# Kernel tuning notes

Measured on AMD Instinct MI355X. Metric: run time of the kernel, lower is better.

## Reference

```python
import jax, jax.numpy as jnp
import numpy as np

B, T, N, H, L, KS = 8, 1024, 64, 8, 2, 3  # batch, seq_len, num_features(=graph n), heads, blocks, Cheb order
D1 = 64  # tq MLP hidden (hardcoded 64 in original)
EPS = 1e-6


def setup_inputs() -> dict:
    key = jax.random.key(0)
    ks = jax.random.split(key, 30)
    def nrm(k, shp, sc=0.05):
        return jax.random.normal(k, shp, dtype=jnp.float32) * sc
    return {
        "inputs": jax.random.normal(ks[0], (B, T, N), dtype=jnp.float32),
        "pos_emb": nrm(ks[1], (T, N)),
        "K3": nrm(ks[2], (N, KS, N), 0.1),  # Chebyshev kernel Lk reshaped [n, Ks, n] (constant)
        "qw": nrm(ks[3], (L, H, KS)), "qb": nrm(ks[4], (L, H)),
        "kw": nrm(ks[5], (L, H, KS)), "kb": nrm(ks[6], (L, H)),
        "vw": nrm(ks[7], (L, H, KS)), "vb": nrm(ks[8], (L, H)),
        "tqW1": nrm(ks[9], (L, H, T, D1)), "tqb1": nrm(ks[10], (L, H, D1)),
        "tqW2": nrm(ks[11], (L, H, D1, D1)), "tqb2": nrm(ks[12], (L, H, D1)),
        "tqW3": nrm(ks[13], (L, H, D1, 2)), "tqb3": nrm(ks[14], (L, H, 2)),
        "Wlt": nrm(ks[15], (L, H * N, N)),
        "ln1g": jnp.ones((L, N), jnp.float32), "ln1b": jnp.zeros((L, N), jnp.float32),
        "ln2g": jnp.ones((L, N), jnp.float32), "ln2b": jnp.zeros((L, N), jnp.float32),
        "sclw": nrm(ks[16], (L, KS)), "sclb": nrm(ks[17], (L,)),
        "elW": nrm(ks[18], (L, N, N)), "elb": nrm(ks[19], (L, N)),
        "fW1": nrm(ks[20], (N, 32)), "fb1": nrm(ks[21], (32,)),
        "fW2": nrm(ks[22], (32, 1)), "fb2": nrm(ks[23], (1,)),
    }


def _ln(x, g, b):
    m = jnp.mean(x, axis=-1, keepdims=True)
    v = jnp.mean((x - m) ** 2, axis=-1, keepdims=True)
    return (x - m) * jax.lax.rsqrt(v + EPS) * g + b


def _head_gconv(x, K3, ws, bs):
    # SpatialConvLayer (c_in=c_out=1) per head: relu(sum_k ws[h,k]*(x @ L_k) + bs[h] + x)
    g = jnp.einsum('btn,nkm,hk->bhtm', x, K3, ws) + bs[None, :, None, None]
    return jax.nn.relu(g + x[:, None])  # [B,H,T,N]


def reference(inputs, pos_emb, K3, qw, qb, kw, kb, vw, vb, tqW1, tqb1, tqW2, tqb2,
              tqW3, tqb3, Wlt, ln1g, ln1b, ln2g, ln2b, sclw, sclb, elW, elb,
              fW1, fb1, fW2, fb2):
    x = inputs + pos_emb  # position embedding layer
    for l in range(L):
        xq = _head_gconv(x, K3, qw[l], qb[l])
        xk = _head_gconv(x, K3, kw[l], kb[l])
        xv = _head_gconv(x, K3, vw[l], vb[l])
        # s_a[b,t,s] = sum_n xk[b,t,n] * xq[b,s,n], scaled by 1/num_features
        s = jnp.einsum('bhtn,bhsn->bhts', xk, xq) / N
        sft = jax.nn.softmax(s, axis=-1)
        # talking-quantity gate: MLP over rows of transposed softmax matrix
        p = jnp.swapaxes(sft, -1, -2)  # [B,H,T,T]
        h1 = jax.nn.relu(jnp.einsum('bhts,hsd->bhtd', p, tqW1[l]) + tqb1[l][None, :, None, :])
        h2 = jax.nn.relu(jnp.einsum('bhtd,hde->bhte', h1, tqW2[l]) + tqb2[l][None, :, None, :])
        g = jax.nn.softmax(jnp.einsum('bhtd,hde->bhte', h2, tqW3[l]) + tqb3[l][None, :, None, :], axis=-1)  # [B,H,T,2]
        auv = jnp.einsum('bhts,bhsn->bhtn', sft, xv)
        ho = g[..., 0:1] * auv + g[..., 1:2] * xv  # gated mix, [B,H,T,N]
        a_x = jnp.transpose(ho, (0, 2, 1, 3)).reshape(B, T, H * N)  # head concat
        out1 = _ln(x + a_x @ Wlt[l], ln1g[l], ln1b[l])  # dropout omitted (inference)
        gc = jnp.einsum('btn,nkm,k->btm', out1, K3, sclw[l]) + sclb[l]
        ffn = jax.nn.relu(gc + out1)  # SpatialConvLayer residual relu
        ffn = ffn @ elW[l] + elb[l]
        x = _ln(out1 + ffn, ln2g[l], ln2b[l])
    pooled = jnp.mean(x, axis=1)  # GlobalAveragePooling1D
    h = jax.nn.relu(pooled @ fW1 + fb1)
    return h @ fW2 + fb2  # [B,1]
```

## Files before the change

### kernel.cpp

```cpp
#include <hip/hip_runtime.h>

typedef __attribute__((ext_vector_type(8))) short short8;
typedef __attribute__((ext_vector_type(4))) float f32x4;

#define BB 8
#define TT 1024
#define NN 64
#define HH 8
#define LL 2
#define KSS 3
#define DD1 64
#define EPSV 1e-6f
#define LOG2E 1.4426950408889634f

#define MFMA16(a, b, c) __builtin_amdgcn_mfma_f32_16x16x32_bf16(a, b, c, 0, 0, 0)
#define BAR() __builtin_amdgcn_s_barrier()
#define WAIT_VM8() asm volatile("s_waitcnt vmcnt(8)" ::: "memory")
#define WAIT_VM2() asm volatile("s_waitcnt vmcnt(2)" ::: "memory")
#define WAIT_VM0() asm volatile("s_waitcnt vmcnt(0)" ::: "memory")
#define WAIT_LGKM0() asm volatile("s_waitcnt lgkmcnt(0)" ::: "memory")

__device__ __forceinline__ float exp2_(float x) { return __builtin_amdgcn_exp2f(x); }
__device__ __forceinline__ float log2_(float x) { return __builtin_amdgcn_logf(x); }

__device__ __forceinline__ void split1(float x, ushort& hi, ushort& lo) {
  uint u = __float_as_uint(x);
  hi = (ushort)(u >> 16);
  float hf = __uint_as_float(u & 0xffff0000u);
  lo = (ushort)(__float_as_uint(x - hf) >> 16);
}
__device__ __forceinline__ uint pack2(float a, float b, uint& lo) {
  uint ua = __float_as_uint(a), ub = __float_as_uint(b);
  float ra = __uint_as_float(ua & 0xffff0000u);
  float rb = __uint_as_float(ub & 0xffff0000u);
  lo = (__float_as_uint(a - ra) >> 16) | (__float_as_uint(b - rb) & 0xffff0000u);
  return (ua >> 16) | (ub & 0xffff0000u);
}
__device__ __forceinline__ uint pack2rhu(float a, float b) {
  uint ua = __float_as_uint(a) + 0x8000u;
  uint ub = __float_as_uint(b) + 0x8000u;
  return (ua >> 16) | (ub & 0xffff0000u);
}
__device__ __forceinline__ ushort f2bfr(float x) {
  union { float f; uint u; } v; v.f = x;
  uint r = (v.u + 0x7fffu + ((v.u >> 16) & 1u)) >> 16;
  return (ushort)r;
}
__device__ __forceinline__ float bf2f(ushort b) {
  union { uint u; float f; } v; v.u = ((uint)b) << 16; return v.f;
}

__device__ __forceinline__ void gl2lds16(const ushort* g, ushort* l) {
  __builtin_amdgcn_global_load_lds(
      (const __attribute__((address_space(1))) void*)g,
      (__attribute__((address_space(3))) void*)l, 16, 0, 0);
}
__device__ __forceinline__ void stage_async(ushort* __restrict__ s,
                                            const ushort* __restrict__ g,
                                            int stride, int tid) {
  int w = tid >> 6;
  int sub = (tid & 63) >> 3, c = tid & 7;
#pragma unroll
  for (int i = 0; i < 2; ++i) {
    int rb = (i * 4 + w) * 8;
    gl2lds16(g + (size_t)(rb + sub) * stride + ((c ^ sub) << 3), s + rb * 64);
  }
}
__device__ __forceinline__ short8 frag(const ushort* __restrict__ s, int row, int ch) {
  return *(const short8*)(s + row * 64 + ((ch ^ (row & 7)) << 3));
}
__device__ __forceinline__ void stage_q32(ushort* __restrict__ s,
                                          const ushort* __restrict__ g, int tid) {
  int w = tid >> 6;
  int sub = (tid & 63) >> 3, c = tid & 7;
  int rb = w * 8, r = rb + sub;
  gl2lds16(g + (size_t)r * 64 + ((c ^ (r & 7)) << 3), s + rb * 64);
}
__device__ __forceinline__ void stage_v32(ushort* __restrict__ s,
                                          const ushort* __restrict__ g, int tid) {
  int w = tid >> 6;
  int noff = (tid & 63) >> 2, c = tid & 3;
  int nb = w * 16, n = nb + noff;
  gl2lds16(g + (size_t)n * 1024 + ((c ^ ((n >> 1) & 3)) << 3), s + nb * 32);
}
__device__ __forceinline__ short8 frag32(const ushort* __restrict__ s, int row, int g) {
  return *(const short8*)(s + row * 32 + ((g ^ ((row >> 1) & 3)) << 3));
}


__global__ void k_addpos(const float* __restrict__ in, const float* __restrict__ pe,
                         float* __restrict__ x, int total) {
  int idx = blockIdx.x * 256 + threadIdx.x;
  if (idx < total) {
    int tn = idx & (TT * NN - 1);
    x[idx] = in[idx] + pe[tn];
  }
}

__global__ void k_k3s(const float* __restrict__ K3, const float* __restrict__ sclwl,
                      ushort* __restrict__ dh) {
  int idx = blockIdx.x * 256 + threadIdx.x;
  int n = idx >> 6, m = idx & 63;
  float v = K3[n * 192 + m] * sclwl[0] + K3[n * 192 + 64 + m] * sclwl[1] +
            K3[n * 192 + 128 + m] * sclwl[2];
  dh[m * 64 + n] = f2bfr(v);
}

__global__ __launch_bounds__(256) void k_tsplit(const float* __restrict__ src,
                                                ushort* __restrict__ dh) {
  __shared__ float st[64][65];
  int blk = blockIdx.x;
  int mat = blk >> 4, rt = blk & 15;
  int tid = threadIdx.x;
  size_t sbase = ((size_t)mat * TT + rt * 64) * 64;
#pragma unroll
  for (int i = 0; i < 4; ++i) {
    int idx = tid + i * 256;
    int r = idx >> 4, c4 = idx & 15;
    float4 v = *(const float4*)(src + sbase + r * 64 + c4 * 4);
    st[r][c4 * 4 + 0] = v.x; st[r][c4 * 4 + 1] = v.y;
    st[r][c4 * 4 + 2] = v.z; st[r][c4 * 4 + 3] = v.w;
  }
  __syncthreads();
  size_t obase = (size_t)mat * (64 * (size_t)TT) + rt * 64;
#pragma unroll
  for (int i = 0; i < 2; ++i) {
    int idx = tid + i * 256;
    int n = idx >> 3, c = idx & 7;
    uint hw[4];
#pragma unroll
    for (int j = 0; j < 4; ++j)
      hw[j] = (uint)f2bfr(st[c * 8 + 2 * j][n]) | ((uint)f2bfr(st[c * 8 + 2 * j + 1][n]) << 16);
    *(uint4*)(dh + obase + (size_t)n * TT + c * 8) = make_uint4(hw[0], hw[1], hw[2], hw[3]);
  }
}

__global__ __launch_bounds__(256) void k_tsplitW(const float* __restrict__ Wlt,
                                                 ushort* __restrict__ dh,
                                                 ushort* __restrict__ dl) {
  __shared__ float st[64][65];
  int blk = blockIdx.x;
  int l = blk >> 3, rt = blk & 7;
  int tid = threadIdx.x;
  size_t sbase = ((size_t)l * 512 + rt * 64) * 64;
#pragma unroll
  for (int i = 0; i < 4; ++i) {
    int idx = tid + i * 256;
    int r = idx >> 4, c4 = idx & 15;
    float4 v = *(const float4*)(Wlt + sbase + r * 64 + c4 * 4);
    st[r][c4 * 4 + 0] = v.x; st[r][c4 * 4 + 1] = v.y;
    st[r][c4 * 4 + 2] = v.z; st[r][c4 * 4 + 3] = v.w;
  }
  __syncthreads();
  size_t obase = (size_t)l * 64 * 512 + rt * 64;
#pragma unroll
  for (int i = 0; i < 2; ++i) {
    int idx = tid + i * 256;
    int n = idx >> 3, c = idx & 7;
    uint hw[4], lw[4];
#pragma unroll
    for (int j = 0; j < 4; ++j) hw[j] = pack2(st[c * 8 + 2 * j][n], st[c * 8 + 2 * j + 1][n], lw[j]);
    *(uint4*)(dh + obase + (size_t)n * 512 + c * 8) = make_uint4(hw[0], hw[1], hw[2], hw[3]);
    *(uint4*)(dl + obase + (size_t)n * 512 + c * 8) = make_uint4(lw[0], lw[1], lw[2], lw[3]);
  }
}

__global__ __launch_bounds__(256) void k_tsplitSq(const float* __restrict__ src,
                                                  ushort* __restrict__ dh) {
  __shared__ float st[64][65];
  int mat = blockIdx.x;
  int tid = threadIdx.x;
  size_t sbase = (size_t)mat * 4096;
#pragma unroll
  for (int i = 0; i < 4; ++i) {
    int idx = tid + i * 256;
    int r = idx >> 4, c4 = idx & 15;
    float4 v = *(const float4*)(src + sbase + r * 64 + c4 * 4);
    st[r][c4 * 4 + 0] = v.x; st[r][c4 * 4 + 1] = v.y;
    st[r][c4 * 4 + 2] = v.z; st[r][c4 * 4 + 3] = v.w;
  }
  __syncthreads();
#pragma unroll
  for (int i = 0; i < 2; ++i) {
    int idx = tid + i * 256;
    int d = idx >> 3, c = idx & 7;
    uint hw[4];
#pragma unroll
    for (int j = 0; j < 4; ++j)
      hw[j] = (uint)f2bfr(st[c * 8 + 2 * j][d]) | ((uint)f2bfr(st[c * 8 + 2 * j + 1][d]) << 16);
    *(uint4*)(dh + sbase + (size_t)d * 64 + c * 8) = make_uint4(hw[0], hw[1], hw[2], hw[3]);
  }
}

__global__ __launch_bounds__(256) void k_gconv(
    const float* __restrict__ x, const float* __restrict__ K3,
    const float* __restrict__ qwl, const float* __restrict__ qbl,
    const float* __restrict__ kwl, const float* __restrict__ kbl,
    const float* __restrict__ vwl, const float* __restrict__ vbl,
    ushort* __restrict__ xqh, ushort* __restrict__ xkh, float* __restrict__ xv) {
  __shared__ float sK3[12288];
  __shared__ float sx[4][64];
  int tid = threadIdx.x;
  int w = tid >> 6, lane = tid & 63;
#pragma unroll
  for (int i = 0; i < 12; ++i)
    ((float4*)sK3)[tid + i * 256] = ((const float4*)K3)[tid + i * 256];
  size_t bt = (size_t)blockIdx.x * 4 + w;
  size_t b = bt >> 10, t = bt & 1023;
  float xm = x[bt * 64 + lane];
  sx[w][lane] = xm;
  __syncthreads();
  float a0 = 0.f, a1 = 0.f, a2 = 0.f;
#pragma unroll 8
  for (int n = 0; n < 64; ++n) {
    float xn = sx[w][n];
    a0 = fmaf(xn, sK3[n * 192 + lane], a0);
    a1 = fmaf(xn, sK3[n * 192 + 64 + lane], a1);
    a2 = fmaf(xn, sK3[n * 192 + 128 + lane], a2);
  }
#pragma unroll
  for (int hh = 0; hh < HH; ++hh) {
    size_t off = (((size_t)b * HH + hh) * TT + t) * 64 + lane;
    float q = fmaf(qwl[hh * 3 + 0], a0,
              fmaf(qwl[hh * 3 + 1], a1, fmaf(qwl[hh * 3 + 2], a2, qbl[hh] + xm)));
    q = fmaxf(q, 0.f) * (0.015625f * LOG2E);
    xqh[off] = f2bfr(q);
    float k = fmaf(kwl[hh * 3 + 0], a0,
              fmaf(kwl[hh * 3 + 1], a1, fmaf(kwl[hh * 3 + 2], a2, kbl[hh] + xm)));
    xkh[off] = f2bfr(fmaxf(k, 0.f));
    float v = fmaf(vwl[hh * 3 + 0], a0,
              fmaf(vwl[hh * 3 + 1], a1, fmaf(vwl[hh * 3 + 2], a2, vbl[hh] + xm)));
    xv[off] = fmaxf(v, 0.f);
  }
}

__global__ __launch_bounds__(256, 4) void k_attn(
    const ushort* __restrict__ xkh, const ushort* __restrict__ xqh,
    const ushort* __restrict__ xvTh,
    float* __restrict__ auv, float* __restrict__ lse) {
  __shared__ ushort sQh[4096];
  __shared__ ushort sVh[4096];
  __shared__ ushort sPh[2048];
  int tid = threadIdx.x;
  int lane = tid & 63, w = tid >> 6;
  int l15 = lane & 15, g = lane >> 4;
  int nb = gridDim.x, chunk = nb >> 3, bid = blockIdx.x;
  int blk = (bid & 7) * chunk + (bid >> 3);
  int bh = blk >> 4, t0 = (blk & 15) << 6;
  size_t bhTT = (size_t)bh * TT;
  int trow = 16 * w + l15, psw = (trow >> 1) & 3;

  stage_async(sQh, xkh + (bhTT + t0) * NN, 64, tid);
  WAIT_VM0();
  BAR();
  short8 fKh[2];
#pragma unroll
  for (int ks = 0; ks < 2; ++ks) fKh[ks] = frag(sQh, trow, g + 4 * ks);
  WAIT_LGKM0();
  BAR();
  stage_q32(sQh, xqh + bhTT * NN, tid);
  stage_v32(sVh, xvTh + bhTT * NN, tid);
  stage_q32(sQh + 2048, xqh + (bhTT + 32) * NN, tid);
  stage_v32(sVh + 2048, xvTh + bhTT * NN + 32, tid);

  float lsum = 0.f;
  f32x4 O[4];
#pragma unroll
  for (int ct = 0; ct < 4; ++ct)
#pragma unroll
    for (int r = 0; r < 4; ++r) O[ct][r] = 0.f;

  for (int ut = 0; ut < 32; ++ut) {
    int cur = ut & 1;
    if (ut < 31) WAIT_VM2(); else WAIT_VM0();
    BAR();
    const ushort* cQh = sQh + cur * 2048;
    const ushort* cVh = sVh + cur * 2048;

    __builtin_amdgcn_s_setprio(1);
    f32x4 S[2];
#pragma unroll
    for (int rt = 0; rt < 2; ++rt) {
      f32x4 a = {0.f, 0.f, 0.f, 0.f};
#pragma unroll
      for (int ks = 0; ks < 2; ++ks)
        a = MFMA16(frag(cQh, 16 * rt + l15, g + 4 * ks), fKh[ks], a);
      S[rt] = a;
    }
    __builtin_amdgcn_s_setprio(0);

    uint2 ph[2];
#pragma unroll
    for (int rt = 0; rt < 2; ++rt) {
      float p0 = exp2_(S[rt][0]), p1 = exp2_(S[rt][1]);
      float p2 = exp2_(S[rt][2]), p3 = exp2_(S[rt][3]);
      lsum += (p0 + p1) + (p2 + p3);
      ph[rt].x = pack2rhu(p0, p1);
      ph[rt].y = pack2rhu(p2, p3);
    }
#pragma unroll
    for (int rt = 0; rt < 2; ++rt) {
      int ch = 2 * rt + (g >> 1);
      int off = trow * 32 + ((ch ^ psw) << 3) + ((g & 1) << 2);
      *(uint2*)(sPh + off) = ph[rt];
    }
    WAIT_LGKM0();
    __builtin_amdgcn_sched_barrier(0);
    __builtin_amdgcn_s_setprio(1);
    {
      short8 aPh = frag32(sPh, trow, g);
#pragma unroll
      for (int ct = 0; ct < 4; ++ct)
        O[ct] = MFMA16(aPh, frag32(cVh, 16 * ct + l15, g), O[ct]);
    }
    __builtin_amdgcn_s_setprio(0);
    WAIT_LGKM0();
    BAR();
    if (ut < 30) {
      int tn = ut + 2;
      stage_q32(sQh + cur * 2048, xqh + (bhTT + tn * 32) * NN, tid);
      stage_v32(sVh + cur * 2048, xvTh + bhTT * NN + tn * 32, tid);
    }
  }
  lsum += __shfl_xor(lsum, 16, 64);
  lsum += __shfl_xor(lsum, 32, 64);
  float il = 1.0f / lsum;
  float ilr[4];
#pragma unroll
  for (int r = 0; r < 4; ++r) ilr[r] = __shfl(il, (lane & 48) | (4 * g + r), 64);
#pragma unroll
  for (int r = 0; r < 4; ++r) {
    size_t row = (bhTT + t0 + 16 * w + 4 * g + r) * NN;
#pragma unroll
    for (int ct = 0; ct < 4; ++ct) auv[row + 16 * ct + l15] = O[ct][r] * ilr[r];
  }
  if (g == 0) lse[bhTT + t0 + trow] = log2_(lsum);
}

__global__ __launch_bounds__(256, 4) void k_h1g(
    const ushort* __restrict__ xkh, const ushort* __restrict__ xqh,
    const ushort* __restrict__ w1Th, const float* __restrict__ lse,
    const float* __restrict__ b1, const ushort* __restrict__ w2Th,
    const float* __restrict__ b2l, const float* __restrict__ W3l,
    const float* __restrict__ b3l, const float* __restrict__ auv,
    const float* __restrict__ xv, ushort* __restrict__ hoh,
    ushort* __restrict__ hol) {
  __shared__ ushort sKh[4096];
  __shared__ ushort sWh[4096];
  __shared__ ushort sPh[2048];
  __shared__ ushort sW2[4096];
  __shared__ float sL[1024];
  int tid = threadIdx.x;
  int lane = tid & 63, w = tid >> 6;
  int l15 = lane & 15, g = lane >> 4;
  int nb = gridDim.x, chunk = nb >> 3, bid = blockIdx.x;
  int blk = (bid & 7) * chunk + (bid >> 3);
  int bh = blk >> 4, h = bh & (HH - 1), a0 = (blk & 15) << 6;
  size_t bhTT = (size_t)bh * TT;
  size_t wbase = (size_t)h * NN * TT;
  int arow = 16 * w + l15, psw = (arow >> 1) & 3;

  stage_async(sKh, xqh + (bhTT + a0) * NN, 64, tid);
  stage_async(sW2, w2Th + (size_t)h * 4096, 64, tid);
  WAIT_VM0();
  BAR();
  short8 fQh[2];
#pragma unroll
  for (int ks = 0; ks < 2; ++ks) fQh[ks] = frag(sKh, arow, g + 4 * ks);
#pragma unroll
  for (int i = 0; i < 4; ++i) sL[tid + i * 256] = lse[bhTT + tid + i * 256];
  WAIT_LGKM0();
  BAR();
  stage_q32(sKh, xkh + bhTT * NN, tid);
  stage_v32(sWh, w1Th + wbase, tid);
  stage_q32(sKh + 2048, xkh + (bhTT + 32) * NN, tid);
  stage_v32(sWh + 2048, w1Th + wbase + 32, tid);

  f32x4 acc[4];
#pragma unroll
  for (int ct = 0; ct < 4; ++ct)
#pragma unroll
    for (int r = 0; r < 4; ++r) acc[ct][r] = 0.f;

  for (int tt = 0; tt < 32; ++tt) {
    int cur = tt & 1;
    if (tt < 31) WAIT_VM2(); else WAIT_VM0();
    BAR();
    const ushort* cKh = sKh + cur * 2048;
    const ushort* cWh = sWh + cur * 2048;

    __builtin_amdgcn_s_setprio(1);
    f32x4 S[2];
#pragma unroll
    for (int rt = 0; rt < 2; ++rt) {
      f32x4 a = {0.f, 0.f, 0.f, 0.f};
#pragma unroll
      for (int ks = 0; ks < 2; ++ks)
        a = MFMA16(frag(cKh, 16 * rt + l15, g + 4 * ks), fQh[ks], a);
      S[rt] = a;
    }
    __builtin_amdgcn_s_setprio(0);

    uint2 ph[2];
#pragma unroll
    for (int rt = 0; rt < 2; ++rt) {
      f32x4 lv = *(const f32x4*)(sL + tt * 32 + 16 * rt + 4 * g);
      float p0 = exp2_(S[rt][0] - lv[0]);
      float p1 = exp2_(S[rt][1] - lv[1]);
      float p2 = exp2_(S[rt][2] - lv[2]);
      float p3 = exp2_(S[rt][3] - lv[3]);
      ph[rt].x = pack2rhu(p0, p1);
      ph[rt].y = pack2rhu(p2, p3);
    }
#pragma unroll
    for (int rt = 0; rt < 2; ++rt) {
      int ch = 2 * rt + (g >> 1);
      int off = arow * 32 + ((ch ^ psw) << 3) + ((g & 1) << 2);
      *(uint2*)(sPh + off) = ph[rt];
    }
    WAIT_LGKM0();
    __builtin_amdgcn_sched_barrier(0);
    __builtin_amdgcn_s_setprio(1);
    {
      short8 aPh = frag32(sPh, arow, g);
#pragma unroll
      for (int ct = 0; ct < 4; ++ct)
        acc[ct] = MFMA16(aPh, frag32(cWh, 16 * ct + l15, g), acc[ct]);
    }
    __builtin_amdgcn_s_setprio(0);
    WAIT_LGKM0();
    BAR();
    if (tt < 30) {
      int tn = tt + 2;
      stage_q32(sKh + cur * 2048, xkh + (bhTT + tn * 32) * NN, tid);
      stage_v32(sWh + cur * 2048, w1Th + wbase + tn * 32, tid);
    }
  }
#pragma unroll
  for (int ct = 0; ct < 4; ++ct) {
    float bb = b1[h * 64 + 16 * ct + l15];
    int cch = 2 * ct + (l15 >> 3), cin = l15 & 7;
#pragma unroll
    for (int r = 0; r < 4; ++r) {
      int row = 16 * w + 4 * g + r;
      float hv = fmaxf(acc[ct][r] + bb, 0.f);
      sWh[row * 64 + ((cch ^ (row & 7)) << 3) + cin] = f2bfr(hv);
    }
  }
  WAIT_LGKM0();
  BAR();
  f32x4 acc2[4];
#pragma unroll
  for (int rt = 0; rt < 4; ++rt)
#pragma unroll
    for (int r = 0; r < 4; ++r) acc2[rt][r] = 0.f;
#pragma unroll
  for (int ks = 0; ks < 2; ++ks) {
    short8 bB = frag(sW2, 16 * w + l15, g + 4 * ks);
#pragma unroll
    for (int rt = 0; rt < 4; ++rt)
      acc2[rt] = MFMA16(frag(sWh, 16 * rt + l15, g + 4 * ks), bB, acc2[rt]);
  }
  int col = 16 * w + l15;
  float b2c = b2l[h * 64 + col];
  float w30 = W3l[h * 128 + col * 2 + 0];
  float w31 = W3l[h * 128 + col * 2 + 1];
  float* sredf = sL;
  float* sgf = sL + 512;
#pragma unroll
  for (int rt = 0; rt < 4; ++rt)
#pragma unroll
    for (int r = 0; r < 4; ++r) {
      float v = fmaxf(acc2[rt][r] + b2c, 0.f);
      float z0 = v * w30, z1 = v * w31;
#pragma unroll
      for (int mm = 1; mm < 16; mm <<= 1) {
        z0 += __shfl_xor(z0, mm, 64);
        z1 += __shfl_xor(z1, mm, 64);
      }
      if (l15 == 0) {
        int row = 16 * rt + 4 * g + r;
        sredf[row * 4 + w] = z0;
        sredf[256 + row * 4 + w] = z1;
      }
    }
  __syncthreads();
  if (tid < 64) {
    float z0 = sredf[tid * 4] + sredf[tid * 4 + 1] + sredf[tid * 4 + 2] +
               sredf[tid * 4 + 3] + b3l[h * 2 + 0];
    float z1 = sredf[256 + tid * 4] + sredf[256 + tid * 4 + 1] +
               sredf[256 + tid * 4 + 2] + sredf[256 + tid * 4 + 3] + b3l[h * 2 + 1];
    float g0 = 1.0f / (1.0f + __expf(z1 - z0));
    sgf[tid * 2] = g0;
    sgf[tid * 2 + 1] = 1.0f - g0;
  }
  __syncthreads();
#pragma unroll
  for (int rr = 0; rr < 16; ++rr) {
    int row = 16 * w + rr;
    size_t off = (bhTT + a0 + row) * 64 + lane;
    float ho = sgf[row * 2] * auv[off] + sgf[row * 2 + 1] * xv[off];
    ushort hb, lb;
    split1(ho, hb, lb);
    hoh[off] = hb;
    hol[off] = lb;
  }
}

__global__ __launch_bounds__(256, 2) void k_mrgf(
    float* __restrict__ x, const ushort* __restrict__ hoh,
    const ushort* __restrict__ hol, const ushort* __restrict__ wth,
    const ushort* __restrict__ wtl, const float* __restrict__ g1l,
    const float* __restrict__ b1l, const float* __restrict__ sclb_l,
    const ushort* __restrict__ k3sTh, const ushort* __restrict__ elWTh,
    const float* __restrict__ elbl, const float* __restrict__ g2l,
    const float* __restrict__ b2l) {
  __shared__ ushort sAh[2][4096], sAl[2][4096], sBh[2][4096], sBl[2][4096];
  __shared__ float sred[2][64][4];
  __shared__ float sfin[64][2];
  int tid = threadIdx.x;
  int lane = tid & 63, w = tid >> 6;
  int l15 = lane & 15, g = lane >> 4;
  int blk = blockIdx.x;
  int b = blk >> 4, t0 = (blk & 15) << 6;

  {
    size_t ab0 = (((size_t)b * HH + 0) * TT + t0) * NN;
    size_t ab1 = (((size_t)b * HH + 1) * TT + t0) * NN;
    stage_async(sAh[0], hoh + ab0, 64, tid);
    stage_async(sAl[0], hol + ab0, 64, tid);
    stage_async(sBh[0], wth, 512, tid);
    stage_async(sBl[0], wtl, 512, tid);
    stage_async(sAh[1], hoh + ab1, 64, tid);
    stage_async(sAl[1], hol + ab1, 64, tid);
    stage_async(sBh[1], wth + 64, 512, tid);
    stage_async(sBl[1], wtl + 64, 512, tid);
  }

  f32x4 acc[4];
#pragma unroll
  for (int rt = 0; rt < 4; ++rt)
#pragma unroll
    for (int r = 0; r < 4; ++r) acc[rt][r] = 0.f;

  for (int h = 0; h < 8; ++h) {
    int cur = h & 1;
    if (h < 7) WAIT_VM8(); else WAIT_VM0();
    BAR();
    __builtin_amdgcn_s_setprio(1);
#pragma unroll
    for (int ks = 0; ks < 2; ++ks) {
      short8 bBh = frag(sBh[cur], 16 * w + l15, g + 4 * ks);
      short8 bBl = frag(sBl[cur], 16 * w + l15, g + 4 * ks);
#pragma unroll
      for (int rt = 0; rt < 4; ++rt) {
        short8 aAh = frag(sAh[cur], 16 * rt + l15, g + 4 * ks);
        short8 aAl = frag(sAl[cur], 16 * rt + l15, g + 4 * ks);
        acc[rt] = MFMA16(aAh, bBh, acc[rt]);
        acc[rt] = MFMA16(aAh, bBl, acc[rt]);
        acc[rt] = MFMA16(aAl, bBh, acc[rt]);
      }
    }
    __builtin_amdgcn_s_setprio(0);
    WAIT_LGKM0();
    BAR();
    if (h < 6) {
      int hn = h + 2;
      size_t ab = (((size_t)b * HH + hn) * TT + t0) * NN;
      stage_async(sAh[cur], hoh + ab, 64, tid);
      stage_async(sAl[cur], hol + ab, 64, tid);
      stage_async(sBh[cur], wth + hn * 64, 512, tid);
      stage_async(sBl[cur], wtl + hn * 64, 512, tid);
    }
  }
  stage_async(sBh[0], k3sTh, 64, tid);
  stage_async(sBl[0], elWTh, 64, tid);
  int mcol = 16 * w + l15;
  float vv[4][4];
#pragma unroll
  for (int rt = 0; rt < 4; ++rt)
#pragma unroll
    for (int r = 0; r < 4; ++r) {
      int row = 16 * rt + 4 * g + r;
      vv[rt][r] = acc[rt][r] + x[((size_t)b * TT + t0 + row) * 64 + mcol];
    }
#pragma unroll
  for (int rt = 0; rt < 4; ++rt)
#pragma unroll
    for (int r = 0; r < 4; ++r) {
      float s1 = vv[rt][r], s2 = vv[rt][r] * vv[rt][r];
#pragma unroll
      for (int mm = 1; mm < 16; mm <<= 1) {
        s1 += __shfl_xor(s1, mm, 64);
        s2 += __shfl_xor(s2, mm, 64);
      }
      if (l15 == 0) {
        int row = 16 * rt + 4 * g + r;
        sred[0][row][w] = s1;
        sred[1][row][w] = s2;
      }
    }
  __syncthreads();
  if (tid < 64) {
    float a1 = sred[0][tid][0] + sred[0][tid][1] + sred[0][tid][2] + sred[0][tid][3];
    float a2 = sred[1][tid][0] + sred[1][tid][1] + sred[1][tid][2] + sred[1][tid][3];
    float mean = a1 * (1.0f / 64.0f);
    float var = a2 * (1.0f / 64.0f) - mean * mean;
    sfin[tid][0] = mean;
    sfin[tid][1] = rsqrtf(var + EPSV);
  }
  __syncthreads();
  float gg = g1l[mcol], bb1 = b1l[mcol];
  float val[4][4];
  ushort* sH = sAh[0];
  ushort* sHl = sAl[0];
  int cch = mcol >> 3, cin = mcol & 7;
#pragma unroll
  for (int rt = 0; rt < 4; ++rt)
#pragma unroll
    for (int r = 0; r < 4; ++r) {
      int row = 16 * rt + 4 * g + r;
      float v = (vv[rt][r] - sfin[row][0]) * sfin[row][1] * gg + bb1;
      val[rt][r] = v;
      ushort hb, lb;
      split1(v, hb, lb);
      int a = row * 64 + ((cch ^ (row & 7)) << 3) + cin;
      sH[a] = hb;
      sHl[a] = lb;
    }
  WAIT_VM0();
  WAIT_LGKM0();
  BAR();
  f32x4 acc3[4];
#pragma unroll
  for (int rt = 0; rt < 4; ++rt)
#pragma unroll
    for (int r = 0; r < 4; ++r) acc3[rt][r] = 0.f;
#pragma unroll
  for (int ks = 0; ks < 2; ++ks) {
    short8 bB = frag(sBh[0], mcol, g + 4 * ks);
#pragma unroll
    for (int rt = 0; rt < 4; ++rt) {
      acc3[rt] = MFMA16(frag(sH, 16 * rt + l15, g + 4 * ks), bB, acc3[rt]);
      acc3[rt] = MFMA16(frag(sHl, 16 * rt + l15, g + 4 * ks), bB, acc3[rt]);
    }
  }
  WAIT_LGKM0();
  BAR();
  float sclb = sclb_l[0];
#pragma unroll
  for (int rt = 0; rt < 4; ++rt)
#pragma unroll
    for (int r = 0; r < 4; ++r) {
      int row = 16 * rt + 4 * g + r;
      float f1 = fmaxf(acc3[rt][r] + sclb + val[rt][r], 0.f);
      ushort hb, lb;
      split1(f1, hb, lb);
      int a = row * 64 + ((cch ^ (row & 7)) << 3) + cin;
      sH[a] = hb;
      sHl[a] = lb;
    }
  WAIT_LGKM0();
  BAR();
  f32x4 acc4[4];
#pragma unroll
  for (int rt = 0; rt < 4; ++rt)
#pragma unroll
    for (int r = 0; r < 4; ++r) acc4[rt][r] = 0.f;
#pragma unroll
  for (int ks = 0; ks < 2; ++ks) {
    short8 bB = frag(sBl[0], mcol, g + 4 * ks);
#pragma unroll
    for (int rt = 0; rt < 4; ++rt) {
      acc4[rt] = MFMA16(frag(sH, 16 * rt + l15, g + 4 * ks), bB, acc4[rt]);
      acc4[rt] = MFMA16(frag(sHl, 16 * rt + l15, g + 4 * ks), bB, acc4[rt]);
    }
  }
  float elb = elbl[mcol];
#pragma unroll
  for (int rt = 0; rt < 4; ++rt)
#pragma unroll
    for (int r = 0; r < 4; ++r) {
      float v = val[rt][r] + acc4[rt][r] + elb;
      vv[rt][r] = v;
      float s1 = v, s2 = v * v;
#pragma unroll
      for (int mm = 1; mm < 16; mm <<= 1) {
        s1 += __shfl_xor(s1, mm, 64);
        s2 += __shfl_xor(s2, mm, 64);
      }
      if (l15 == 0) {
        int row = 16 * rt + 4 * g + r;
        sred[0][row][w] = s1;
        sred[1][row][w] = s2;
      }
    }
  __syncthreads();
  if (tid < 64) {
    float a1 = sred[0][tid][0] + sred[0][tid][1] + sred[0][tid][2] + sred[0][tid][3];
    float a2 = sred[1][tid][0] + sred[1][tid][1] + sred[1][tid][2] + sred[1][tid][3];
    float mean = a1 * (1.0f / 64.0f);
    float var = a2 * (1.0f / 64.0f) - mean * mean;
    sfin[tid][0] = mean;
    sfin[tid][1] = rsqrtf(var + EPSV);
  }
  __syncthreads();
  float g2 = g2l[mcol], bb2 = b2l[mcol];
#pragma unroll
  for (int rt = 0; rt < 4; ++rt)
#pragma unroll
    for (int r = 0; r < 4; ++r) {
      int row = 16 * rt + 4 * g + r;
      x[((size_t)b * TT + t0 + row) * 64 + mcol] =
          (vv[rt][r] - sfin[row][0]) * sfin[row][1] * g2 + bb2;
    }
}

__global__ __launch_bounds__(256) void k_final(
    const float* __restrict__ x, const float* __restrict__ fW1,
    const float* __restrict__ fb1, const float* __restrict__ fW2,
    const float* __restrict__ fb2, float* __restrict__ out) {
  __shared__ float pl[4][64];
  int tid = threadIdx.x;
  int lane = tid & 63, w = tid >> 6;
  size_t b = blockIdx.x;
  float s = 0.f;
  for (int t = 256 * w; t < 256 * w + 256; ++t) s += x[(b * TT + t) * 64 + lane];
  pl[w][lane] = s;
  __syncthreads();
  if (tid < 64) pl[0][tid] = (pl[0][tid] + pl[1][tid] + pl[2][tid] + pl[3][tid]) * (1.0f / TT);
  __syncthreads();
  if (tid < 64) {
    float hv = 0.f;
    if (lane < 32) {
      hv = fb1[lane];
#pragma unroll 8
      for (int n = 0; n < 64; ++n) hv = fmaf(pl[0][n], fW1[n * 32 + lane], hv);
      hv = fmaxf(hv, 0.f) * fW2[lane];
    }
#pragma unroll
    for (int m = 1; m < 64; m <<= 1) hv += __shfl_xor(hv, m, 64);
    if (lane == 0) out[b] = hv + fb2[0];
  }
}

extern "C" void kernel_launch(void* const* d_in, const int* in_sizes, int n_in,
                              void* d_out, int out_size, void* d_ws, size_t ws_size,
                              hipStream_t stream) {
  const float* inputs = (const float*)d_in[0];
  const float* pos_emb = (const float*)d_in[1];
  const float* K3 = (const float*)d_in[2];
  const float* qw = (const float*)d_in[3];
  const float* qb = (const float*)d_in[4];
  const float* kw = (const float*)d_in[5];
  const float* kb = (const float*)d_in[6];
  const float* vw = (const float*)d_in[7];
  const float* vb = (const float*)d_in[8];
  const float* tqW1 = (const float*)d_in[9];
  const float* tqb1 = (const float*)d_in[10];
  const float* tqW2 = (const float*)d_in[11];
  const float* tqb2 = (const float*)d_in[12];
  const float* tqW3 = (const float*)d_in[13];
  const float* tqb3 = (const float*)d_in[14];
  const float* Wlt = (const float*)d_in[15];
  const float* ln1g = (const float*)d_in[16];
  const float* ln1b = (const float*)d_in[17];
  const float* ln2g = (const float*)d_in[18];
  const float* ln2b = (const float*)d_in[19];
  const float* sclw = (const float*)d_in[20];
  const float* sclb = (const float*)d_in[21];
  const float* elW = (const float*)d_in[22];
  const float* elb = (const float*)d_in[23];
  const float* fW1 = (const float*)d_in[24];
  const float* fb1 = (const float*)d_in[25];
  const float* fW2 = (const float*)d_in[26];
  const float* fb2 = (const float*)d_in[27];
  float* out = (float*)d_out;
  float* ws_f = (float*)d_ws;

  const size_t TN = (size_t)TT * NN;
  const size_t HTN = (size_t)HH * TT * NN;
  const size_t W1T_ELEMS = (size_t)LL * HH * NN * TT;
  const size_t WLT_ELEMS = (size_t)LL * 64 * 512;

  ushort* k3sTh = (ushort*)ws_f;
  ushort* w1Th = k3sTh + (size_t)LL * 4096;
  ushort* wth = w1Th + W1T_ELEMS;
  ushort* wtl = wth + WLT_ELEMS;
  ushort* w2Th = wtl + WLT_ELEMS;
  ushort* elWTh = w2Th + (size_t)LL * HH * 4096;
  size_t base_ush = (size_t)LL * 4096 + W1T_ELEMS + 2 * WLT_ELEMS +
                    (size_t)LL * HH * 4096 + (size_t)LL * 4096;
  const size_t base = (base_ush + 1) / 2;

  for (int l = 0; l < LL; ++l)
    k_k3s<<<16, 256, 0, stream>>>(K3, sclw + l * KSS, k3sTh + (size_t)l * 4096);
  k_tsplit<<<LL * HH * 16, 256, 0, stream>>>(tqW1, w1Th);
  k_tsplitW<<<LL * 8, 256, 0, stream>>>(Wlt, wth, wtl);
  k_tsplitSq<<<LL * HH, 256, 0, stream>>>(tqW2, w2Th);
  k_tsplitSq<<<LL, 256, 0, stream>>>(elW, elWTh);

  const size_t per_b = TN + 2 * HTN + (size_t)HH * TT + (5 * HTN) / 2;
  size_t avail = ws_size / sizeof(float);
  avail = (avail > base) ? avail - base : 0;
  int Bc = (int)(avail / per_b);
  if (Bc > BB) Bc = BB;
  if (Bc < 1) Bc = 1;

  for (int b0 = 0; b0 < BB; b0 += Bc) {
    int bc = (BB - b0 < Bc) ? (BB - b0) : Bc;
    float* x = ws_f + base;
    float* xv = x + (size_t)bc * TN;
    float* auv = xv + (size_t)bc * HTN;
    float* lseb = auv + (size_t)bc * HTN;
    ushort* xqh = (ushort*)(lseb + (size_t)bc * HH * TT);
    ushort* xkh = xqh + (size_t)bc * HTN;
    ushort* xvTh = xkh + (size_t)bc * HTN;
    ushort* hoh = xvTh + (size_t)bc * HTN;
    ushort* hol = hoh + (size_t)bc * HTN;

    int total = bc * (int)TN;
    k_addpos<<<(total + 255) / 256, 256, 0, stream>>>(inputs + (size_t)b0 * TN, pos_emb, x,
                                                      total);
    for (int l = 0; l < LL; ++l) {
      k_gconv<<<bc * TT / 4, 256, 0, stream>>>(x, K3, qw + l * HH * KSS, qb + l * HH,
                                               kw + l * HH * KSS, kb + l * HH,
                                               vw + l * HH * KSS, vb + l * HH,
                                               xqh, xkh, xv);
      k_tsplit<<<bc * HH * 16, 256, 0, stream>>>(xv, xvTh);
      k_attn<<<bc * HH * 16, 256, 0, stream>>>(xkh, xqh, xvTh, auv, lseb);
      k_h1g<<<bc * HH * 16, 256, 0, stream>>>(
          xkh, xqh, w1Th + (size_t)l * HH * NN * TT, lseb, tqb1 + l * HH * DD1,
          w2Th + (size_t)l * HH * 4096, tqb2 + l * HH * DD1,
          tqW3 + (size_t)l * HH * DD1 * 2, tqb3 + l * HH * 2, auv, xv, hoh, hol);
      k_mrgf<<<bc * 16, 256, 0, stream>>>(
          x, hoh, hol, wth + (size_t)l * 64 * 512, wtl + (size_t)l * 64 * 512,
          ln1g + l * NN, ln1b + l * NN, sclb + l, k3sTh + (size_t)l * 4096,
          elWTh + (size_t)l * 4096, elb + l * NN, ln2g + l * NN, ln2b + l * NN);
    }
    k_final<<<bc, 256, 0, stream>>>(x, fW1, fb1, fW2, fb2, out + b0);
  }
}
```

Baseline: 245.7 us.

## Split attention key range across two blocks and halve merge-kernel row tiles

The attention kernel now splits the 1024-key loop into two halves handled by separate blocks. Each block writes unnormalized partial outputs and partial sums to separate buffers, and the gate kernel combines them, applying the log and reciprocal normalization there. The merge/FFN kernel also processes 32 rows per block instead of 64, doubling its grid. Both changes aim to raise parallelism and occupancy, at the cost of extra global traffic for the second partial-output buffer and more workspace per batch.

```diff
diff --git a/kernel.cpp b/kernel.cpp
--- a/kernel.cpp
+++ b/kernel.cpp
@@ -15,7 +15,7 @@
 
 #define MFMA16(a, b, c) __builtin_amdgcn_mfma_f32_16x16x32_bf16(a, b, c, 0, 0, 0)
 #define BAR() __builtin_amdgcn_s_barrier()
-#define WAIT_VM8() asm volatile("s_waitcnt vmcnt(8)" ::: "memory")
+#define WAIT_VM6() asm volatile("s_waitcnt vmcnt(6)" ::: "memory")
 #define WAIT_VM2() asm volatile("s_waitcnt vmcnt(2)" ::: "memory")
 #define WAIT_VM0() asm volatile("s_waitcnt vmcnt(0)" ::: "memory")
 #define WAIT_LGKM0() asm volatile("s_waitcnt lgkmcnt(0)" ::: "memory")
@@ -234,10 +234,11 @@
   }
 }
 
-__global__ __launch_bounds__(256, 4) void k_attn(
+__global__ __launch_bounds__(256) void k_attn(
     const ushort* __restrict__ xkh, const ushort* __restrict__ xqh,
     const ushort* __restrict__ xvTh,
-    float* __restrict__ auv, float* __restrict__ lse) {
+    float* __restrict__ auv0, float* __restrict__ auv1,
+    float* __restrict__ ls0, float* __restrict__ ls1) {
   __shared__ ushort sQh[4096];
   __shared__ ushort sVh[4096];
   __shared__ ushort sPh[2048];
@@ -246,8 +247,9 @@
   int l15 = lane & 15, g = lane >> 4;
   int nb = gridDim.x, chunk = nb >> 3, bid = blockIdx.x;
   int blk = (bid & 7) * chunk + (bid >> 3);
-  int bh = blk >> 4, t0 = (blk & 15) << 6;
+  int bh = blk >> 5, t0 = ((blk >> 1) & 15) << 6, half = blk & 1;
   size_t bhTT = (size_t)bh * TT;
+  size_t ubase = (size_t)(half << 9);
   int trow = 16 * w + l15, psw = (trow >> 1) & 3;
 
   stage_async(sQh, xkh + (bhTT + t0) * NN, 64, tid);
@@ -258,10 +260,10 @@
   for (int ks = 0; ks < 2; ++ks) fKh[ks] = frag(sQh, trow, g + 4 * ks);
   WAIT_LGKM0();
   BAR();
-  stage_q32(sQh, xqh + bhTT * NN, tid);
-  stage_v32(sVh, xvTh + bhTT * NN, tid);
-  stage_q32(sQh + 2048, xqh + (bhTT + 32) * NN, tid);
-  stage_v32(sVh + 2048, xvTh + bhTT * NN + 32, tid);
+  stage_q32(sQh, xqh + (bhTT + ubase) * NN, tid);
+  stage_v32(sVh, xvTh + bhTT * NN + ubase, tid);
+  stage_q32(sQh + 2048, xqh + (bhTT + ubase + 32) * NN, tid);
+  stage_v32(sVh + 2048, xvTh + bhTT * NN + ubase + 32, tid);
 
   float lsum = 0.f;
   f32x4 O[4];
@@ -270,9 +272,9 @@
 #pragma unroll
     for (int r = 0; r < 4; ++r) O[ct][r] = 0.f;
 
-  for (int ut = 0; ut < 32; ++ut) {
+  for (int ut = 0; ut < 16; ++ut) {
     int cur = ut & 1;
-    if (ut < 31) WAIT_VM2(); else WAIT_VM0();
+    if (ut < 15) WAIT_VM2(); else WAIT_VM0();
     BAR();
     const ushort* cQh = sQh + cur * 2048;
     const ushort* cVh = sVh + cur * 2048;
@@ -316,33 +318,33 @@
     __builtin_amdgcn_s_setprio(0);
     WAIT_LGKM0();
     BAR();
-    if (ut < 30) {
+    if (ut < 14) {
       int tn = ut + 2;
-      stage_q32(sQh + cur * 2048, xqh + (bhTT + tn * 32) * NN, tid);
-      stage_v32(sVh + cur * 2048, xvTh + bhTT * NN + tn * 32, tid);
+      stage_q32(sQh + cur * 2048, xqh + (bhTT + ubase + tn * 32) * NN, tid);
+      stage_v32(sVh + cur * 2048, xvTh + bhTT * NN + ubase + tn * 32, tid);
     }
   }
   lsum += __shfl_xor(lsum, 16, 64);
   lsum += __shfl_xor(lsum, 32, 64);
-  float il = 1.0f / lsum;
-  float ilr[4];
-#pragma unroll
-  for (int r = 0; r < 4; ++r) ilr[r] = __shfl(il, (lane & 48) | (4 * g + r), 64);
+  float* A = half ? auv1 : auv0;
+  float* L = half ? ls1 : ls0;
 #pragma unroll
   for (int r = 0; r < 4; ++r) {
     size_t row = (bhTT + t0 + 16 * w + 4 * g + r) * NN;
 #pragma unroll
-    for (int ct = 0; ct < 4; ++ct) auv[row + 16 * ct + l15] = O[ct][r] * ilr[r];
-  }
-  if (g == 0) lse[bhTT + t0 + trow] = log2_(lsum);
+    for (int ct = 0; ct < 4; ++ct) A[row + 16 * ct + l15] = O[ct][r];
+  }
+  if (g == 0) L[bhTT + t0 + trow] = lsum;
 }
 
 __global__ __launch_bounds__(256, 4) void k_h1g(
     const ushort* __restrict__ xkh, const ushort* __restrict__ xqh,
-    const ushort* __restrict__ w1Th, const float* __restrict__ lse,
+    const ushort* __restrict__ w1Th,
+    const float* __restrict__ ls0, const float* __restrict__ ls1,
     const float* __restrict__ b1, const ushort* __restrict__ w2Th,
     const float* __restrict__ b2l, const float* __restrict__ W3l,
-    const float* __restrict__ b3l, const float* __restrict__ auv,
+    const float* __restrict__ b3l,
+    const float* __restrict__ auv0, const float* __restrict__ auv1,
     const float* __restrict__ xv, ushort* __restrict__ hoh,
     ushort* __restrict__ hol) {
   __shared__ ushort sKh[4096];
@@ -350,6 +352,7 @@
   __shared__ ushort sPh[2048];
   __shared__ ushort sW2[4096];
   __shared__ float sL[1024];
+  __shared__ float sIl[1024];
   int tid = threadIdx.x;
   int lane = tid & 63, w = tid >> 6;
   int l15 = lane & 15, g = lane >> 4;
@@ -368,7 +371,12 @@
 #pragma unroll
   for (int ks = 0; ks < 2; ++ks) fQh[ks] = frag(sKh, arow, g + 4 * ks);
 #pragma unroll
-  for (int i = 0; i < 4; ++i) sL[tid + i * 256] = lse[bhTT + tid + i * 256];
+  for (int i = 0; i < 4; ++i) {
+    int idx = tid + i * 256;
+    float l = ls0[bhTT + idx] + ls1[bhTT + idx];
+    sL[idx] = log2_(l);
+    sIl[idx] = 1.0f / l;
+  }
   WAIT_LGKM0();
   BAR();
   stage_q32(sKh, xkh + bhTT * NN, tid);
@@ -491,7 +499,7 @@
     float z1 = sredf[256 + tid * 4] + sredf[256 + tid * 4 + 1] +
                sredf[256 + tid * 4 + 2] + sredf[256 + tid * 4 + 3] + b3l[h * 2 + 1];
     float g0 = 1.0f / (1.0f + __expf(z1 - z0));
-    sgf[tid * 2] = g0;
+    sgf[tid * 2] = g0 * sIl[a0 + tid];
     sgf[tid * 2 + 1] = 1.0f - g0;
   }
   __syncthreads();
@@ -499,7 +507,8 @@
   for (int rr = 0; rr < 16; ++rr) {
     int row = 16 * w + rr;
     size_t off = (bhTT + a0 + row) * 64 + lane;
-    float ho = sgf[row * 2] * auv[off] + sgf[row * 2 + 1] * xv[off];
+    float o = auv0[off] + auv1[off];
+    float ho = sgf[row * 2] * o + sgf[row * 2 + 1] * xv[off];
     ushort hb, lb;
     split1(ho, hb, lb);
     hoh[off] = hb;
@@ -515,37 +524,37 @@
     const ushort* __restrict__ k3sTh, const ushort* __restrict__ elWTh,
     const float* __restrict__ elbl, const float* __restrict__ g2l,
     const float* __restrict__ b2l) {
-  __shared__ ushort sAh[2][4096], sAl[2][4096], sBh[2][4096], sBl[2][4096];
-  __shared__ float sred[2][64][4];
-  __shared__ float sfin[64][2];
+  __shared__ ushort sAh[2][2048], sAl[2][2048], sBh[2][4096], sBl[2][4096];
+  __shared__ float sred[2][32][4];
+  __shared__ float sfin[32][2];
   int tid = threadIdx.x;
   int lane = tid & 63, w = tid >> 6;
   int l15 = lane & 15, g = lane >> 4;
   int blk = blockIdx.x;
-  int b = blk >> 4, t0 = (blk & 15) << 6;
+  int b = blk >> 5, t0 = (blk & 31) << 5;
 
   {
     size_t ab0 = (((size_t)b * HH + 0) * TT + t0) * NN;
     size_t ab1 = (((size_t)b * HH + 1) * TT + t0) * NN;
-    stage_async(sAh[0], hoh + ab0, 64, tid);
-    stage_async(sAl[0], hol + ab0, 64, tid);
+    stage_q32(sAh[0], hoh + ab0, tid);
+    stage_q32(sAl[0], hol + ab0, tid);
     stage_async(sBh[0], wth, 512, tid);
     stage_async(sBl[0], wtl, 512, tid);
-    stage_async(sAh[1], hoh + ab1, 64, tid);
-    stage_async(sAl[1], hol + ab1, 64, tid);
+    stage_q32(sAh[1], hoh + ab1, tid);
+    stage_q32(sAl[1], hol + ab1, tid);
     stage_async(sBh[1], wth + 64, 512, tid);
     stage_async(sBl[1], wtl + 64, 512, tid);
   }
 
-  f32x4 acc[4];
-#pragma unroll
-  for (int rt = 0; rt < 4; ++rt)
+  f32x4 acc[2];
+#pragma unroll
+  for (int rt = 0; rt < 2; ++rt)
 #pragma unroll
     for (int r = 0; r < 4; ++r) acc[rt][r] = 0.f;
 
   for (int h = 0; h < 8; ++h) {
     int cur = h & 1;
-    if (h < 7) WAIT_VM8(); else WAIT_VM0();
+    if (h < 7) WAIT_VM6(); else WAIT_VM0();
     BAR();
     __builtin_amdgcn_s_setprio(1);
 #pragma unroll
@@ -553,7 +562,7 @@
       short8 bBh = frag(sBh[cur], 16 * w + l15, g + 4 * ks);
       short8 bBl = frag(sBl[cur], 16 * w + l15, g + 4 * ks);
 #pragma unroll
-      for (int rt = 0; rt < 4; ++rt) {
+      for (int rt = 0; rt < 2; ++rt) {
         short8 aAh = frag(sAh[cur], 16 * rt + l15, g + 4 * ks);
         short8 aAl = frag(sAl[cur], 16 * rt + l15, g + 4 * ks);
         acc[rt] = MFMA16(aAh, bBh, acc[rt]);
@@ -567,8 +576,8 @@
     if (h < 6) {
       int hn = h + 2;
       size_t ab = (((size_t)b * HH + hn) * TT + t0) * NN;
-      stage_async(sAh[cur], hoh + ab, 64, tid);
-      stage_async(sAl[cur], hol + ab, 64, tid);
+      stage_q32(sAh[cur], hoh + ab, tid);
+      stage_q32(sAl[cur], hol + ab, tid);
       stage_async(sBh[cur], wth + hn * 64, 512, tid);
       stage_async(sBl[cur], wtl + hn * 64, 512, tid);
     }
@@ -576,16 +585,16 @@
   stage_async(sBh[0], k3sTh, 64, tid);
   stage_async(sBl[0], elWTh, 64, tid);
   int mcol = 16 * w + l15;
-  float vv[4][4];
-#pragma unroll
-  for (int rt = 0; rt < 4; ++rt)
+  float vv[2][4];
+#pragma unroll
+  for (int rt = 0; rt < 2; ++rt)
 #pragma unroll
     for (int r = 0; r < 4; ++r) {
       int row = 16 * rt + 4 * g + r;
       vv[rt][r] = acc[rt][r] + x[((size_t)b * TT + t0 + row) * 64 + mcol];
     }
 #pragma unroll
-  for (int rt = 0; rt < 4; ++rt)
+  for (int rt = 0; rt < 2; ++rt)
 #pragma unroll
     for (int r = 0; r < 4; ++r) {
       float s1 = vv[rt][r], s2 = vv[rt][r] * vv[rt][r];
@@ -601,7 +610,7 @@
       }
     }
   __syncthreads();
-  if (tid < 64) {
+  if (tid < 32) {
     float a1 = sred[0][tid][0] + sred[0][tid][1] + sred[0][tid][2] + sred[0][tid][3];
     float a2 = sred[1][tid][0] + sred[1][tid][1] + sred[1][tid][2] + sred[1][tid][3];
     float mean = a1 * (1.0f / 64.0f);
@@ -611,12 +620,12 @@
   }
   __syncthreads();
   float gg = g1l[mcol], bb1 = b1l[mcol];
-  float val[4][4];
+  float val[2][4];
   ushort* sH = sAh[0];
   ushort* sHl = sAl[0];
   int cch = mcol >> 3, cin = mcol & 7;
 #pragma unroll
-  for (int rt = 0; rt < 4; ++rt)
+  for (int rt = 0; rt < 2; ++rt)
 #pragma unroll
     for (int r = 0; r < 4; ++r) {
       int row = 16 * rt + 4 * g + r;
@@ -631,16 +640,16 @@
   WAIT_VM0();
   WAIT_LGKM0();
   BAR();
-  f32x4 acc3[4];
-#pragma unroll
-  for (int rt = 0; rt < 4; ++rt)
+  f32x4 acc3[2];
+#pragma unroll
+  for (int rt = 0; rt < 2; ++rt)
 #pragma unroll
     for (int r = 0; r < 4; ++r) acc3[rt][r] = 0.f;
 #pragma unroll
   for (int ks = 0; ks < 2; ++ks) {
     short8 bB = frag(sBh[0], mcol, g + 4 * ks);
 #pragma unroll
-    for (int rt = 0; rt < 4; ++rt) {
+    for (int rt = 0; rt < 2; ++rt) {
       acc3[rt] = MFMA16(frag(sH, 16 * rt + l15, g + 4 * ks), bB, acc3[rt]);
       acc3[rt] = MFMA16(frag(sHl, 16 * rt + l15, g + 4 * ks), bB, acc3[rt]);
     }
@@ -649,7 +658,7 @@
   BAR();
   float sclb = sclb_l[0];
 #pragma unroll
-  for (int rt = 0; rt < 4; ++rt)
+  for (int rt = 0; rt < 2; ++rt)
 #pragma unroll
     for (int r = 0; r < 4; ++r) {
       int row = 16 * rt + 4 * g + r;
@@ -662,23 +671,23 @@
     }
   WAIT_LGKM0();
   BAR();
-  f32x4 acc4[4];
-#pragma unroll
-  for (int rt = 0; rt < 4; ++rt)
+  f32x4 acc4[2];
+#pragma unroll
+  for (int rt = 0; rt < 2; ++rt)
 #pragma unroll
     for (int r = 0; r < 4; ++r) acc4[rt][r] = 0.f;
 #pragma unroll
   for (int ks = 0; ks < 2; ++ks) {
     short8 bB = frag(sBl[0], mcol, g + 4 * ks);
 #pragma unroll
-    for (int rt = 0; rt < 4; ++rt) {
+    for (int rt = 0; rt < 2; ++rt) {
       acc4[rt] = MFMA16(frag(sH, 16 * rt + l15, g + 4 * ks), bB, acc4[rt]);
       acc4[rt] = MFMA16(frag(sHl, 16 * rt + l15, g + 4 * ks), bB, acc4[rt]);
     }
   }
   float elb = elbl[mcol];
 #pragma unroll
-  for (int rt = 0; rt < 4; ++rt)
+  for (int rt = 0; rt < 2; ++rt)
 #pragma unroll
     for (int r = 0; r < 4; ++r) {
       float v = val[rt][r] + acc4[rt][r] + elb;
@@ -696,7 +705,7 @@
       }
     }
   __syncthreads();
-  if (tid < 64) {
+  if (tid < 32) {
     float a1 = sred[0][tid][0] + sred[0][tid][1] + sred[0][tid][2] + sred[0][tid][3];
     float a2 = sred[1][tid][0] + sred[1][tid][1] + sred[1][tid][2] + sred[1][tid][3];
     float mean = a1 * (1.0f / 64.0f);
@@ -707,7 +716,7 @@
   __syncthreads();
   float g2 = g2l[mcol], bb2 = b2l[mcol];
 #pragma unroll
-  for (int rt = 0; rt < 4; ++rt)
+  for (int rt = 0; rt < 2; ++rt)
 #pragma unroll
     for (int r = 0; r < 4; ++r) {
       int row = 16 * rt + 4 * g + r;
@@ -800,7 +809,7 @@
   k_tsplitSq<<<LL * HH, 256, 0, stream>>>(tqW2, w2Th);
   k_tsplitSq<<<LL, 256, 0, stream>>>(elW, elWTh);
 
-  const size_t per_b = TN + 2 * HTN + (size_t)HH * TT + (5 * HTN) / 2;
+  const size_t per_b = TN + 3 * HTN + 2 * (size_t)HH * TT + (5 * HTN) / 2;
   size_t avail = ws_size / sizeof(float);
   avail = (avail > base) ? avail - base : 0;
   int Bc = (int)(avail / per_b);
@@ -811,9 +820,11 @@
     int bc = (BB - b0 < Bc) ? (BB - b0) : Bc;
     float* x = ws_f + base;
     float* xv = x + (size_t)bc * TN;
-    float* auv = xv + (size_t)bc * HTN;
-    float* lseb = auv + (size_t)bc * HTN;
-    ushort* xqh = (ushort*)(lseb + (size_t)bc * HH * TT);
+    float* auv0 = xv + (size_t)bc * HTN;
+    float* auv1 = auv0 + (size_t)bc * HTN;
+    float* ls0 = auv1 + (size_t)bc * HTN;
+    float* ls1 = ls0 + (size_t)bc * HH * TT;
+    ushort* xqh = (ushort*)(ls1 + (size_t)bc * HH * TT);
     ushort* xkh = xqh + (size_t)bc * HTN;
     ushort* xvTh = xkh + (size_t)bc * HTN;
     ushort* hoh = xvTh + (size_t)bc * HTN;
@@ -828,12 +839,13 @@
                                                vw + l * HH * KSS, vb + l * HH,
                                                xqh, xkh, xv);
       k_tsplit<<<bc * HH * 16, 256, 0, stream>>>(xv, xvTh);
-      k_attn<<<bc * HH * 16, 256, 0, stream>>>(xkh, xqh, xvTh, auv, lseb);
+      k_attn<<<bc * HH * 32, 256, 0, stream>>>(xkh, xqh, xvTh, auv0, auv1, ls0, ls1);
       k_h1g<<<bc * HH * 16, 256, 0, stream>>>(
-          xkh, xqh, w1Th + (size_t)l * HH * NN * TT, lseb, tqb1 + l * HH * DD1,
-          w2Th + (size_t)l * HH * 4096, tqb2 + l * HH * DD1,
-          tqW3 + (size_t)l * HH * DD1 * 2, tqb3 + l * HH * 2, auv, xv, hoh, hol);
-      k_mrgf<<<bc * 16, 256, 0, stream>>>(
+          xkh, xqh, w1Th + (size_t)l * HH * NN * TT, ls0, ls1,
+          tqb1 + l * HH * DD1, w2Th + (size_t)l * HH * 4096, tqb2 + l * HH * DD1,
+          tqW3 + (size_t)l * HH * DD1 * 2, tqb3 + l * HH * 2, auv0, auv1, xv,
+          hoh, hol);
+      k_mrgf<<<bc * 32, 256, 0, stream>>>(
           x, hoh, hol, wth + (size_t)l * 64 * 512, wtl + (size_t)l * 64 * 512,
           ln1g + l * NN, ln1b + l * NN, sclb + l, k3sTh + (size_t)l * 4096,
           elWTh + (size_t)l * 4096, elb + l * NN, ln2g + l * NN, ln2b + l * NN);
```

New measurement: 243.8 us. No clear change (-0.8%).
